# Optimization experiments

Measured on AMD Instinct MI355X. Metric: run time of the kernel, lower is better.

## Reference

```python
import jax, jax.numpy as jnp
import numpy as np

N, E, P, D = 100000, 800000, 100000, 128

def setup_inputs() -> dict:
    key = jax.random.key(0)
    ks = jax.random.split(key, 24)
    def w(k, i, o):
        return jax.random.normal(k, (i, o), jnp.float32) * (1.0 / np.sqrt(i))
    inp = {
        'x': jax.random.normal(ks[0], (N, D), jnp.float32),
        'src': jax.random.randint(ks[1], (E,), 0, N, jnp.int32),
        'dst': jax.random.randint(ks[2], (E,), 0, N, jnp.int32),
        'pos_src': jax.random.randint(ks[3], (P,), 0, N, jnp.int32),
        'pos_dst': jax.random.randint(ks[4], (P,), 0, N, jnp.int32),
        'neg_src': jax.random.randint(ks[5], (P,), 0, N, jnp.int32),
        'neg_dst': jax.random.randint(ks[6], (P,), 0, N, jnp.int32),
        # SAGEConv params: fc_self, fc_neigh (+bias) per layer
        'Ws0': w(ks[7], D, D), 'Wn0': w(ks[8], D, D), 'b0': jnp.zeros((D,), jnp.float32),
        'Ws1': w(ks[9], D, D), 'Wn1': w(ks[10], D, D), 'b1': jnp.zeros((D,), jnp.float32),
        'Ws2': w(ks[11], D, D), 'Wn2': w(ks[12], D, D), 'b2': jnp.zeros((D,), jnp.float32),
        # predictor MLP: D->D->D->2
        'Wp0': w(ks[13], D, D), 'bp0': jnp.zeros((D,), jnp.float32),
        'Wp1': w(ks[14], D, D), 'bp1': jnp.zeros((D,), jnp.float32),
        'Wp2': w(ks[15], D, 2), 'bp2': jnp.zeros((2,), jnp.float32),
    }
    return inp

def _sage_layer(h, src, dst, n, Ws, Wn, b, act):
    # mean aggregation over in-neighbors (gather -> segment_sum -> divide)
    msum = jax.ops.segment_sum(h[src], dst, num_segments=n)      # [N, D]
    deg = jax.ops.segment_sum(jnp.ones_like(dst, jnp.float32), dst, num_segments=n)
    h_neigh = msum / jnp.maximum(deg, 1.0)[:, None]
    out = h @ Ws + h_neigh @ Wn + b
    return jax.nn.relu(out) if act else out

def _predict(hs, hd, Wp0, bp0, Wp1, bp1, Wp2, bp2):
    z = hs * hd
    z = jax.nn.relu(z @ Wp0 + bp0)
    z = jax.nn.relu(z @ Wp1 + bp1)
    return jax.nn.softmax(z @ Wp2 + bp2, axis=1)[:, 1]

def reference(x, src, dst, pos_src, pos_dst, neg_src, neg_dst,
              Ws0, Wn0, b0, Ws1, Wn1, b1, Ws2, Wn2, b2,
              Wp0, bp0, Wp1, bp1, Wp2, bp2):
    n = x.shape[0]
    h = _sage_layer(x, src, dst, n, Ws0, Wn0, b0, True)
    h = _sage_layer(h, src, dst, n, Ws1, Wn1, b1, True)
    h = _sage_layer(h, src, dst, n, Ws2, Wn2, b2, False)
    pos = _predict(h[pos_src], h[pos_dst], Wp0, bp0, Wp1, bp1, Wp2, bp2)
    neg = _predict(h[neg_src], h[neg_dst], Wp0, bp0, Wp1, bp1, Wp2, bp2)
    return (pos, neg)
```

## Files before the change

kernel.cpp:

```cpp
#include <hip/hip_runtime.h>
#include <cstdint>
#include <cstddef>
#include <cmath>

#define D 128

typedef short bf16x8 __attribute__((ext_vector_type(8)));
typedef float f32x4 __attribute__((ext_vector_type(4)));

__device__ __forceinline__ ushort f2b(float f) {
  uint x = __float_as_uint(f);
  uint r = ((x >> 16) & 1u) + 0x7fffu;
  return (ushort)((x + r) >> 16);
}
__device__ __forceinline__ float b2f(ushort u) {
  return __uint_as_float(((uint)u) << 16);
}

__global__ __launch_bounds__(256) void k_degree_p(const int* __restrict__ dst, int E,
    int* __restrict__ deg, float scale, int CE) {
  int part = blockIdx.x & 7, chunk = blockIdx.x >> 3;
  long base = (long)chunk * CE;
  for (int i = threadIdx.x; i < CE; i += 256) {
    long e = base + i;
    if (e < E) {
      int d = dst[e];
      int p = (int)((float)d * scale); if (p > 7) p = 7;
      if (p == part) atomicAdd(&deg[d], 1);
    }
  }
}

__global__ __launch_bounds__(256) void k_fill_p(const int* __restrict__ src,
    const int* __restrict__ dst, int E, int* __restrict__ cursor,
    int* __restrict__ csrc, float scale, int CE) {
  int part = blockIdx.x & 7, chunk = blockIdx.x >> 3;
  long base = (long)chunk * CE;
  for (int i = threadIdx.x; i < CE; i += 256) {
    long e = base + i;
    if (e < E) {
      int d = dst[e];
      int p = (int)((float)d * scale); if (p > 7) p = 7;
      if (p == part) {
        int s = src[e];
        int pos = atomicAdd(&cursor[d], 1);
        csrc[pos] = s;
      }
    }
  }
}

#define SCAN_T 256
#define SCAN_E 4
#define SCAN_CHUNK (SCAN_T * SCAN_E)

__global__ void k_scan_partial(const int* __restrict__ deg, int n, int* __restrict__ part) {
  __shared__ int s[SCAN_T];
  int base = blockIdx.x * SCAN_CHUNK;
  int sum = 0;
  for (int i = 0; i < SCAN_E; ++i) {
    int idx = base + (int)threadIdx.x * SCAN_E + i;
    if (idx < n) sum += deg[idx];
  }
  s[threadIdx.x] = sum; __syncthreads();
  for (int ofs = SCAN_T / 2; ofs > 0; ofs >>= 1) {
    if ((int)threadIdx.x < ofs) s[threadIdx.x] += s[threadIdx.x + ofs];
    __syncthreads();
  }
  if (threadIdx.x == 0) part[blockIdx.x] = s[0];
}

__global__ void k_scan_part_ex(int* __restrict__ part, int nb) {
  __shared__ int s[1024];
  int v = ((int)threadIdx.x < nb) ? part[threadIdx.x] : 0;
  s[threadIdx.x] = v; __syncthreads();
  for (int ofs = 1; ofs < 1024; ofs <<= 1) {
    int t = ((int)threadIdx.x >= ofs) ? s[threadIdx.x - ofs] : 0;
    __syncthreads();
    s[threadIdx.x] += t;
    __syncthreads();
  }
  if ((int)threadIdx.x < nb) part[threadIdx.x] = s[threadIdx.x] - v;
}

__global__ void k_scan_final(const int* __restrict__ deg, int n, const int* __restrict__ part,
                             int* __restrict__ rowptr, int* __restrict__ cursor, int E) {
  __shared__ int s[SCAN_T];
  int base = blockIdx.x * SCAN_CHUNK;
  int v[SCAN_E]; int local = 0;
  for (int i = 0; i < SCAN_E; ++i) {
    int idx = base + (int)threadIdx.x * SCAN_E + i;
    v[i] = (idx < n) ? deg[idx] : 0;
    local += v[i];
  }
  s[threadIdx.x] = local; __syncthreads();
  for (int ofs = 1; ofs < SCAN_T; ofs <<= 1) {
    int t = ((int)threadIdx.x >= ofs) ? s[threadIdx.x - ofs] : 0;
    __syncthreads();
    s[threadIdx.x] += t;
    __syncthreads();
  }
  int run = part[blockIdx.x] + s[threadIdx.x] - local;
  for (int i = 0; i < SCAN_E; ++i) {
    int idx = base + (int)threadIdx.x * SCAN_E + i;
    if (idx < n) { rowptr[idx] = run; cursor[idx] = run; }
    run += v[i];
  }
  if (blockIdx.x == 0 && threadIdx.x == 0) rowptr[n] = E;
}

__global__ void k_conv_bf16(const float* __restrict__ in, ushort* __restrict__ out, int n8) {
  int i = blockIdx.x * 256 + threadIdx.x;
  if (i >= n8) return;
  float4 a = ((const float4*)in)[i * 2];
  float4 b = ((const float4*)in)[i * 2 + 1];
  ushort4 o0 = {f2b(a.x), f2b(a.y), f2b(a.z), f2b(a.w)};
  ushort4 o1 = {f2b(b.x), f2b(b.y), f2b(b.z), f2b(b.w)};
  ((ushort4*)out)[i * 2] = o0;
  ((ushort4*)out)[i * 2 + 1] = o1;
}

__global__ void k_pack_all(
    const float* __restrict__ Ws0, const float* __restrict__ Wn0,
    const float* __restrict__ Ws1, const float* __restrict__ Wn1,
    const float* __restrict__ Ws2, const float* __restrict__ Wn2,
    const float* __restrict__ Wp0, const float* __restrict__ Wp1,
    ushort* __restrict__ BpL0, ushort* __restrict__ BpL1, ushort* __restrict__ BpL2,
    ushort* __restrict__ BpP0, ushort* __restrict__ BpP1) {
  int o = blockIdx.x * 256 + threadIdx.x;
  const float *W0, *W1; ushort* out; int rel;
  if (o < 32768)       { W0 = Ws0; W1 = Wn0; out = BpL0; rel = o; }
  else if (o < 65536)  { W0 = Ws1; W1 = Wn1; out = BpL1; rel = o - 32768; }
  else if (o < 98304)  { W0 = Ws2; W1 = Wn2; out = BpL2; rel = o - 65536; }
  else if (o < 114688) { W0 = Wp0; W1 = Wp0; out = BpP0; rel = o - 98304; }
  else                 { W0 = Wp1; W1 = Wp1; out = BpP1; rel = o - 114688; }
  int j = rel & 7, lane = (rel >> 3) & 63, t = (rel >> 9) & 7, ks = rel >> 12;
  int k = ks * 32 + ((lane >> 4) * 8) + j;
  int n = t * 16 + (lane & 15);
  const float* W = (k < 128) ? W0 : W1;
  int kk = (k < 128) ? k : k - 128;
  out[rel] = f2b(W[(size_t)kk * D + n]);
}

#define SMS 136
__global__ __launch_bounds__(128, 4) void k_sage_fused(
    const ushort* __restrict__ A, const int* __restrict__ rowptr,
    const int* __restrict__ csrc, const ushort* __restrict__ Bp,
    const float* __restrict__ bias, ushort* __restrict__ out, int N, int do_relu) {
  __shared__ __align__(16) ushort smean[2][16][SMS];
  int tid = threadIdx.x, wave = tid >> 6, lane = tid & 63;
  int m = lane & 15, kg = lane >> 4;
  int g = kg, sub = m;
  int gb = g << 4;
  int row0 = (blockIdx.x * 2 + wave) * 16;
  uint hbo = (uint)(sub * 16);

  int node0 = row0 + g * 4;
  int rpv = 0;
  if (sub < 5) { int ix = node0 + sub; if (ix > N) ix = N; rpv = rowptr[ix]; }
  int beg[4], dgf[4], dd[4];
  #pragma unroll
  for (int j = 0; j < 4; ++j) {
    beg[j] = __shfl(rpv, gb + j);
    int endj = __shfl(rpv, gb + j + 1);
    dgf[j] = endj - beg[j];
    dd[j] = dgf[j] < 16 ? dgf[j] : 16;
  }
  int idxv[4];
  #pragma unroll
  for (int j = 0; j < 4; ++j) {
    int i = beg[j] + sub;
    idxv[j] = (sub < dgf[j]) ? csrc[i] : 0;
  }

  float f[4][8];
  #pragma unroll
  for (int j = 0; j < 4; ++j)
    #pragma unroll
    for (int q = 0; q < 8; ++q) f[j][q] = 0.f;

  int maxdd = dd[0];
  if (dd[1] > maxdd) maxdd = dd[1];
  if (dd[2] > maxdd) maxdd = dd[2];
  if (dd[3] > maxdd) maxdd = dd[3];

  uint off[4][4];
  #pragma unroll
  for (int j = 0; j < 4; ++j)
    #pragma unroll
    for (int k = 0; k < 4; ++k)
      off[j][k] = hbo + ((uint)__shfl(idxv[j], gb + k) << 8);

  #pragma unroll 1
  for (int e = 0; e < maxdd; e += 4) {
    bf16x8 r[4][4];
    #pragma unroll
    for (int j = 0; j < 4; ++j)
      #pragma unroll
      for (int k = 0; k < 4; ++k)
        r[j][k] = *(const bf16x8*)((const char*)A + off[j][k]);
    __builtin_amdgcn_sched_barrier(0);
    #pragma unroll
    for (int j = 0; j < 4; ++j)
      #pragma unroll
      for (int k = 0; k < 4; ++k)
        off[j][k] = hbo + ((uint)__shfl(idxv[j], gb + e + 4 + k) << 8);
    __builtin_amdgcn_sched_barrier(0);
    #pragma unroll
    for (int j = 0; j < 4; ++j) {
      #pragma unroll
      for (int k = 0; k < 4; ++k) {
        float w = (e + k < dd[j]) ? 1.0f : 0.0f;
        #pragma unroll
        for (int q = 0; q < 8; ++q) f[j][q] += w * b2f((ushort)r[j][k][q]);
      }
    }
  }
  #pragma unroll
  for (int j = 0; j < 4; ++j) {
    int endj = beg[j] + dgf[j];
    for (int i = beg[j] + 16; i < endj; ++i) {
      int s = csrc[i];
      bf16x8 v = *(const bf16x8*)((const char*)A + (hbo + ((uint)s << 8)));
      #pragma unroll
      for (int q = 0; q < 8; ++q) f[j][q] += b2f((ushort)v[q]);
    }
  }
  #pragma unroll
  for (int j = 0; j < 4; ++j) {
    float inv = (dgf[j] > 0) ? (1.0f / (float)dgf[j]) : 0.0f;
    bf16x8 o;
    #pragma unroll
    for (int q = 0; q < 8; ++q) o[q] = (short)f2b(f[j][q] * inv);
    *(bf16x8*)&smean[wave][g * 4 + j][sub * 8] = o;
  }
  asm volatile("s_waitcnt lgkmcnt(0)" ::: "memory");
  __builtin_amdgcn_sched_barrier(0);

  int ar = row0 + m; if (ar >= N) ar = N - 1;
  const ushort* a_self = A + (size_t)ar * D + kg * 8;
  f32x4 acc[8];
  #pragma unroll
  for (int t = 0; t < 8; ++t) acc[t] = f32x4{0.f, 0.f, 0.f, 0.f};
  #pragma unroll
  for (int ks = 0; ks < 8; ++ks) {
    bf16x8 af = (ks < 4) ? *(const bf16x8*)(a_self + ks * 32)
                         : *(const bf16x8*)&smean[wave][m][(ks - 4) * 32 + kg * 8];
    const ushort* bb = Bp + (size_t)ks * 4096 + lane * 8;
    #pragma unroll
    for (int t = 0; t < 8; ++t)
      acc[t] = __builtin_amdgcn_mfma_f32_16x16x32_bf16(af, *(const bf16x8*)(bb + t * 512), acc[t], 0, 0, 0);
  }
  #pragma unroll
  for (int t = 0; t < 8; ++t) {
    int c = t * 16 + m;
    float bv = bias[c];
    #pragma unroll
    for (int i = 0; i < 4; ++i) {
      int r = row0 + kg * 4 + i;
      float v = acc[t][i] + bv;
      if (do_relu) v = fmaxf(v, 0.f);
      if (r < N) out[(size_t)r * D + c] = f2b(v);
    }
  }
}

__global__ __launch_bounds__(256) void k_predict_mfma(
    const ushort* __restrict__ h,
    const int* __restrict__ ps, const int* __restrict__ pd,
    const int* __restrict__ ns, const int* __restrict__ nd,
    const ushort* __restrict__ Bp0, const float* __restrict__ bp0,
    const ushort* __restrict__ Bp1, const float* __restrict__ bp1,
    const float* __restrict__ Wp2, const float* __restrict__ bp2,
    float* __restrict__ outp, int P, int pb) {
  __shared__ __align__(16) ushort z1p[4][2048];
  int bi = blockIdx.x;
  const int* sidx; const int* didx; float* op;
  if (bi >= pb) { sidx = ns; didx = nd; op = outp + P; bi -= pb; }
  else          { sidx = ps; didx = pd; op = outp; }
  int tid = threadIdx.x;
  int wave = tid >> 6, lane = tid & 63;
  int m = lane & 15, kg = lane >> 4;
  int pair0 = bi * 64 + wave * 16;
  int prow = pair0 + m; int pr = (prow < P) ? prow : P - 1;
  int si = sidx[pr], di = didx[pr];
  const ushort* hs = h + (size_t)si * D + kg * 8;
  const ushort* hd = h + (size_t)di * D + kg * 8;
  f32x4 acc[8];
  #pragma unroll
  for (int t = 0; t < 8; ++t) acc[t] = f32x4{0.f, 0.f, 0.f, 0.f};
  #pragma unroll
  for (int ks = 0; ks < 4; ++ks) {
    bf16x8 as8 = *(const bf16x8*)(hs + ks * 32);
    bf16x8 ad8 = *(const bf16x8*)(hd + ks * 32);
    bf16x8 af;
    #pragma unroll
    for (int j = 0; j < 8; ++j) {
      float p = b2f((ushort)as8[j]) * b2f((ushort)ad8[j]);
      af[j] = (short)f2b(p);
    }
    const ushort* bb = Bp0 + (size_t)ks * 4096 + lane * 8;
    #pragma unroll
    for (int t = 0; t < 8; ++t)
      acc[t] = __builtin_amdgcn_mfma_f32_16x16x32_bf16(af, *(const bf16x8*)(bb + t * 512), acc[t], 0, 0, 0);
  }
  ushort* zp = &z1p[wave][0];
  #pragma unroll
  for (int t = 0; t < 8; ++t) {
    int c = t * 16 + m;
    float bv = bp0[c];
    int ks2 = c >> 5, kg2 = (c >> 3) & 3, j2 = c & 7;
    #pragma unroll
    for (int i = 0; i < 4; ++i) {
      float v = fmaxf(acc[t][i] + bv, 0.f);
      int l2 = kg2 * 16 + kg * 4 + i;
      zp[(ks2 * 64 + l2) * 8 + j2] = f2b(v);
    }
  }
  __syncthreads();
  #pragma unroll
  for (int t = 0; t < 8; ++t) acc[t] = f32x4{0.f, 0.f, 0.f, 0.f};
  #pragma unroll
  for (int ks = 0; ks < 4; ++ks) {
    bf16x8 af = *(const bf16x8*)(zp + (ks * 64 + lane) * 8);
    const ushort* bb = Bp1 + (size_t)ks * 4096 + lane * 8;
    #pragma unroll
    for (int t = 0; t < 8; ++t)
      acc[t] = __builtin_amdgcn_mfma_f32_16x16x32_bf16(af, *(const bf16x8*)(bb + t * 512), acc[t], 0, 0, 0);
  }
  float p0[4] = {0.f, 0.f, 0.f, 0.f}, p1[4] = {0.f, 0.f, 0.f, 0.f};
  #pragma unroll
  for (int t = 0; t < 8; ++t) {
    int c = t * 16 + m;
    float bv = bp1[c];
    float wa = Wp2[(size_t)c * 2], wb = Wp2[(size_t)c * 2 + 1];
    #pragma unroll
    for (int i = 0; i < 4; ++i) {
      float z = fmaxf(acc[t][i] + bv, 0.f);
      p0[i] += z * wa;
      p1[i] += z * wb;
    }
  }
  #pragma unroll
  for (int msk = 1; msk <= 8; msk <<= 1) {
    #pragma unroll
    for (int i = 0; i < 4; ++i) {
      p0[i] += __shfl_xor(p0[i], msk);
      p1[i] += __shfl_xor(p1[i], msk);
    }
  }
  if (m == 0) {
    float c0 = bp2[0], c1 = bp2[1];
    #pragma unroll
    for (int i = 0; i < 4; ++i) {
      int r = pair0 + kg * 4 + i;
      if (r < P) {
        float l0 = p0[i] + c0, l1 = p1[i] + c1;
        op[r] = 1.0f / (1.0f + expf(l0 - l1));
      }
    }
  }
}

extern "C" void kernel_launch(void* const* d_in, const int* in_sizes, int n_in,
                              void* d_out, int out_size, void* d_ws, size_t ws_size,
                              hipStream_t stream) {
  const float* x       = (const float*)d_in[0];
  const int*   src     = (const int*)d_in[1];
  const int*   dst     = (const int*)d_in[2];
  const int*   pos_src = (const int*)d_in[3];
  const int*   pos_dst = (const int*)d_in[4];
  const int*   neg_src = (const int*)d_in[5];
  const int*   neg_dst = (const int*)d_in[6];
  const float* Ws0 = (const float*)d_in[7],  *Wn0 = (const float*)d_in[8],  *b0 = (const float*)d_in[9];
  const float* Ws1 = (const float*)d_in[10], *Wn1 = (const float*)d_in[11], *b1 = (const float*)d_in[12];
  const float* Ws2 = (const float*)d_in[13], *Wn2 = (const float*)d_in[14], *b2 = (const float*)d_in[15];
  const float* Wp0 = (const float*)d_in[16], *bp0 = (const float*)d_in[17];
  const float* Wp1 = (const float*)d_in[18], *bp1 = (const float*)d_in[19];
  const float* Wp2 = (const float*)d_in[20], *bp2 = (const float*)d_in[21];
  const int N = in_sizes[0] / D;
  const int E = in_sizes[1];
  const int P = in_sizes[3];
  float* outp = (float*)d_out;

  char* ws = (char*)d_ws;
  size_t off = 0;
  auto alloc = [&](size_t bytes) -> void* {
    void* p = ws + off;
    off += (bytes + 255) & ~(size_t)255;
    return p;
  };
  ushort* xb    = (ushort*)alloc((size_t)N * D * 2);
  ushort* h1    = (ushort*)alloc((size_t)N * D * 2);
  ushort* h2    = (ushort*)alloc((size_t)N * D * 2);
  ushort* BpL0  = (ushort*)alloc(256 * D * 2);
  ushort* BpL1  = (ushort*)alloc(256 * D * 2);
  ushort* BpL2  = (ushort*)alloc(256 * D * 2);
  ushort* BpP0  = (ushort*)alloc(128 * D * 2);
  ushort* BpP1  = (ushort*)alloc(128 * D * 2);
  int*    deg    = (int*)alloc((size_t)N * 4);
  int*    rowptr = (int*)alloc((size_t)(N + 1) * 4);
  int*    cursor = (int*)alloc((size_t)N * 4);
  int*    part   = (int*)alloc(4096);
  int*    csrc   = (int*)alloc((size_t)E * 4);
  (void)ws_size; (void)n_in; (void)out_size;

  const float pscale = 8.0f / (float)N;
  const int CB = 96;
  const int CE = (E + CB - 1) / CB;

  hipMemsetAsync(deg, 0, (size_t)N * 4, stream);
  k_degree_p<<<8 * CB, 256, 0, stream>>>(dst, E, deg, pscale, CE);
  int nb = (N + SCAN_CHUNK - 1) / SCAN_CHUNK;
  k_scan_partial<<<nb, SCAN_T, 0, stream>>>(deg, N, part);
  k_scan_part_ex<<<1, 1024, 0, stream>>>(part, nb);
  k_scan_final<<<nb, SCAN_T, 0, stream>>>(deg, N, part, rowptr, cursor, E);
  k_fill_p<<<8 * CB, 256, 0, stream>>>(src, dst, E, cursor, csrc, pscale, CE);

  int n8 = N * D / 8;
  k_conv_bf16<<<(n8 + 255) / 256, 256, 0, stream>>>(x, xb, n8);
  k_pack_all<<<512, 256, 0, stream>>>(Ws0, Wn0, Ws1, Wn1, Ws2, Wn2, Wp0, Wp1,
                                      BpL0, BpL1, BpL2, BpP0, BpP1);

  int gemb = (N + 31) / 32;
  k_sage_fused<<<gemb, 128, 0, stream>>>(xb, rowptr, csrc, BpL0, b0, h1, N, 1);
  k_sage_fused<<<gemb, 128, 0, stream>>>(h1, rowptr, csrc, BpL1, b1, h2, N, 1);
  k_sage_fused<<<gemb, 128, 0, stream>>>(h2, rowptr, csrc, BpL2, b2, xb, N, 0);

  int pb = (P + 63) / 64;
  k_predict_mfma<<<2 * pb, 256, 0, stream>>>(xb, pos_src, pos_dst, neg_src, neg_dst,
                                             BpP0, bp0, BpP1, bp1, Wp2, bp2, outp, P, pb);
}
```

Measured before the change: 440.3 us.

## Gather neighbor rows via global_load_lds into LDS, one edge per step

The neighbor-mean gather now issues direct global-to-LDS loads (global_load_lds, 16 bytes per lane) for one edge slot per iteration. Previously it held 16 in-flight register loads per lane and unrolled four edges per step. Source indices are preloaded in a redistributed layout, and the loop bound is the block-wide max degree, which requires block-level __syncthreads twice per step. The launch-bounds occupancy hint rises from 4 to 6 to cut register pressure and raise occupancy, and the LDS buffer is reused for the mean tile. The trade-off is far fewer bytes in flight per wave and extra barriers, in exchange for fewer VGPRs and more resident waves.

```diff
diff --git a/kernel.cpp b/kernel.cpp
--- a/kernel.cpp
+++ b/kernel.cpp
@@ -15,6 +15,12 @@
 }
 __device__ __forceinline__ float b2f(ushort u) {
   return __uint_as_float(((uint)u) << 16);
+}
+
+__device__ __forceinline__ void gl2lds16(const void* g, void* l) {
+  __builtin_amdgcn_global_load_lds(
+      (__attribute__((address_space(1))) void*)const_cast<void*>(g),
+      (__attribute__((address_space(3))) void*)l, 16, 0, 0);
 }
 
 __global__ __launch_bounds__(256) void k_degree_p(const int* __restrict__ dst, int E,
@@ -143,17 +149,19 @@
 }
 
 #define SMS 136
-__global__ __launch_bounds__(128, 4) void k_sage_fused(
+__global__ __launch_bounds__(128, 6) void k_sage_fused(
     const ushort* __restrict__ A, const int* __restrict__ rowptr,
     const int* __restrict__ csrc, const ushort* __restrict__ Bp,
     const float* __restrict__ bias, ushort* __restrict__ out, int N, int do_relu) {
-  __shared__ __align__(16) ushort smean[2][16][SMS];
+  __shared__ __align__(256) ushort lbuf[2][2176];
+  __shared__ int mdx[2];
   int tid = threadIdx.x, wave = tid >> 6, lane = tid & 63;
   int m = lane & 15, kg = lane >> 4;
   int g = kg, sub = m;
   int gb = g << 4;
   int row0 = (blockIdx.x * 2 + wave) * 16;
-  uint hbo = (uint)(sub * 16);
+  uint slice16 = (uint)(sub * 16);
+  char* lw = (char*)&lbuf[wave][0];
 
   int node0 = row0 + g * 4;
   int rpv = 0;
@@ -166,12 +174,31 @@
     dgf[j] = endj - beg[j];
     dd[j] = dgf[j] < 16 ? dgf[j] : 16;
   }
-  int idxv[4];
-  #pragma unroll
-  for (int j = 0; j < 4; ++j) {
-    int i = beg[j] + sub;
-    idxv[j] = (sub < dgf[j]) ? csrc[i] : 0;
-  }
+
+  int i0 = 0, i1 = 0, i2 = 0, i3 = 0;
+  {
+    int nl = lane >> 2;
+    int hb = ((nl >> 2) << 4) + (nl & 3);
+    int bn = __shfl(rpv, hb);
+    int dn = __shfl(rpv, hb + 1) - bn;
+    int s0 = (lane & 3) << 2;
+    if (s0 + 0 < dn) i0 = csrc[bn + s0 + 0];
+    if (s0 + 1 < dn) i1 = csrc[bn + s0 + 1];
+    if (s0 + 2 < dn) i2 = csrc[bn + s0 + 2];
+    if (s0 + 3 < dn) i3 = csrc[bn + s0 + 3];
+  }
+
+  int md = dd[0];
+  if (dd[1] > md) md = dd[1];
+  if (dd[2] > md) md = dd[2];
+  if (dd[3] > md) md = dd[3];
+  {
+    int t = __shfl_xor(md, 16); if (t > md) md = t;
+    t = __shfl_xor(md, 32); if (t > md) md = t;
+  }
+  if (lane == 0) mdx[wave] = md;
+  __syncthreads();
+  int mdb = mdx[0] > mdx[1] ? mdx[0] : mdx[1];
 
   float f[4][8];
   #pragma unroll
@@ -179,60 +206,48 @@
     #pragma unroll
     for (int q = 0; q < 8; ++q) f[j][q] = 0.f;
 
-  int maxdd = dd[0];
-  if (dd[1] > maxdd) maxdd = dd[1];
-  if (dd[2] > maxdd) maxdd = dd[2];
-  if (dd[3] > maxdd) maxdd = dd[3];
-
-  uint off[4][4];
-  #pragma unroll
-  for (int j = 0; j < 4; ++j)
-    #pragma unroll
-    for (int k = 0; k < 4; ++k)
-      off[j][k] = hbo + ((uint)__shfl(idxv[j], gb + k) << 8);
-
   #pragma unroll 1
-  for (int e = 0; e < maxdd; e += 4) {
-    bf16x8 r[4][4];
-    #pragma unroll
-    for (int j = 0; j < 4; ++j)
+  for (int s = 0; s < mdb; ++s) {
+    {
+      int val = (s & 2) ? ((s & 1) ? i3 : i2) : ((s & 1) ? i1 : i0);
+      int sb = ((lane >> 4) << 2) + (s >> 2);
       #pragma unroll
-      for (int k = 0; k < 4; ++k)
-        r[j][k] = *(const bf16x8*)((const char*)A + off[j][k]);
-    __builtin_amdgcn_sched_barrier(0);
-    #pragma unroll
-    for (int j = 0; j < 4; ++j)
+      for (int q = 0; q < 4; ++q) {
+        int idx = __shfl(val, (q << 4) + sb);
+        gl2lds16((const char*)A + (((uint)idx) << 8) + slice16, lw + (q << 10));
+      }
+    }
+    __syncthreads();
+    const char* rb = lw + g * 1024 + slice16;
+    #pragma unroll
+    for (int j = 0; j < 4; ++j) {
+      bf16x8 v = *(const bf16x8*)(rb + j * 256);
+      float w = (s < dd[j]) ? 1.0f : 0.0f;
       #pragma unroll
-      for (int k = 0; k < 4; ++k)
-        off[j][k] = hbo + ((uint)__shfl(idxv[j], gb + e + 4 + k) << 8);
-    __builtin_amdgcn_sched_barrier(0);
-    #pragma unroll
-    for (int j = 0; j < 4; ++j) {
-      #pragma unroll
-      for (int k = 0; k < 4; ++k) {
-        float w = (e + k < dd[j]) ? 1.0f : 0.0f;
-        #pragma unroll
-        for (int q = 0; q < 8; ++q) f[j][q] += w * b2f((ushort)r[j][k][q]);
-      }
-    }
-  }
+      for (int q = 0; q < 8; ++q) f[j][q] += w * b2f((ushort)v[q]);
+    }
+    __syncthreads();
+  }
+
   #pragma unroll
   for (int j = 0; j < 4; ++j) {
     int endj = beg[j] + dgf[j];
     for (int i = beg[j] + 16; i < endj; ++i) {
-      int s = csrc[i];
-      bf16x8 v = *(const bf16x8*)((const char*)A + (hbo + ((uint)s << 8)));
+      int si = csrc[i];
+      bf16x8 v = *(const bf16x8*)((const char*)A + (((uint)si) << 8) + slice16);
       #pragma unroll
       for (int q = 0; q < 8; ++q) f[j][q] += b2f((ushort)v[q]);
     }
   }
+
+  ushort* smw = (ushort*)lw;
   #pragma unroll
   for (int j = 0; j < 4; ++j) {
     float inv = (dgf[j] > 0) ? (1.0f / (float)dgf[j]) : 0.0f;
     bf16x8 o;
     #pragma unroll
     for (int q = 0; q < 8; ++q) o[q] = (short)f2b(f[j][q] * inv);
-    *(bf16x8*)&smean[wave][g * 4 + j][sub * 8] = o;
+    *(bf16x8*)&smw[(g * 4 + j) * SMS + sub * 8] = o;
   }
   asm volatile("s_waitcnt lgkmcnt(0)" ::: "memory");
   __builtin_amdgcn_sched_barrier(0);
@@ -245,7 +260,7 @@
   #pragma unroll
   for (int ks = 0; ks < 8; ++ks) {
     bf16x8 af = (ks < 4) ? *(const bf16x8*)(a_self + ks * 32)
-                         : *(const bf16x8*)&smean[wave][m][(ks - 4) * 32 + kg * 8];
+                         : *(const bf16x8*)&smw[m * SMS + (ks - 4) * 32 + kg * 8];
     const ushort* bb = Bp + (size_t)ks * 4096 + lane * 8;
     #pragma unroll
     for (int t = 0; t < 8; ++t)
```

New measurement: 451.1 us. 2.4% more time.
